# Optimization experiments

Hardware: AMD Instinct MI355X
Metric: run time of the kernel (lower is better)

Reference implementation:

```python
import jax, jax.numpy as jnp
import numpy as np

B, T, D, H, O = 1024, 512, 64, 64, 32


def setup_inputs() -> dict:
    key = jax.random.key(0)
    ks = jax.random.split(key, 12)
    s = 1.0 / np.sqrt(H)  # torch LSTM/Linear default init scale
    u = lambda k, shape: jax.random.uniform(k, shape, jnp.float32, -s, s)
    return {
        "x": jax.random.normal(ks[0], (B, T, D), jnp.float32),
        # layer 0 (PyTorch gate order: i, f, g, o stacked along first dim)
        "w_ih0": u(ks[1], (4 * H, D)),
        "w_hh0": u(ks[2], (4 * H, H)),
        "b_ih0": u(ks[3], (4 * H,)),
        "b_hh0": u(ks[4], (4 * H,)),
        # layer 1
        "w_ih1": u(ks[5], (4 * H, H)),
        "w_hh1": u(ks[6], (4 * H, H)),
        "b_ih1": u(ks[7], (4 * H,)),
        "b_hh1": u(ks[8], (4 * H,)),
        # final linear head
        "fc_w": u(ks[9], (O, H)),
        "fc_b": u(ks[10], (O,)),
    }


def lstm_layer(x, w_ih, w_hh, b_ih, b_hh):
    """Single batch-first LSTM layer, PyTorch gate order (i, f, g, o)."""
    Bb = x.shape[0]
    Hh = w_hh.shape[1]
    # precompute input contribution for all timesteps: (B, T, 4H)
    pre = jnp.einsum('btd,gd->btg', x, w_ih) + b_ih + b_hh

    def step(carry, p_t):  # p_t: (B, 4H)
        h, c = carry
        gates = p_t + h @ w_hh.T
        i, f, g, o = jnp.split(gates, 4, axis=-1)
        c = jax.nn.sigmoid(f) * c + jax.nn.sigmoid(i) * jnp.tanh(g)
        h = jax.nn.sigmoid(o) * jnp.tanh(c)
        return (h, c), h

    h0 = jnp.zeros((Bb, Hh), x.dtype)
    (_, _), hs = jax.lax.scan(step, (h0, h0), jnp.swapaxes(pre, 0, 1))
    return jnp.swapaxes(hs, 0, 1)  # (B, T, H)


def reference(x, w_ih0, w_hh0, b_ih0, b_hh0, w_ih1, w_hh1, b_ih1, b_hh1, fc_w, fc_b):
    h1 = lstm_layer(x, w_ih0, w_hh0, b_ih0, b_hh0)
    h2 = lstm_layer(h1, w_ih1, w_hh1, b_ih1, b_hh1)
    last = h2[:, -1, :]  # (B, H)
    return jax.nn.softplus(last @ fc_w.T + fc_b)  # (B, O)
```

## Files before the change

kernel.cpp:

```cpp
#include <hip/hip_runtime.h>
#include <math.h>

#define BB 1024
#define TT 512
#define OO 32
#define MM 4
#define NBLK (BB/MM)

typedef __attribute__((ext_vector_type(8))) short short8;
typedef __attribute__((ext_vector_type(4))) float f32x4;

#define MFMA __builtin_amdgcn_mfma_f32_16x16x32_bf16
#define LOG2E 1.4426950408889634f
#define K2    2.8853900817779268f

#define BAR() asm volatile("s_waitcnt lgkmcnt(0)\n\ts_barrier" ::: "memory")

__device__ __forceinline__ float exp2f_(float x) {
#if __has_builtin(__builtin_amdgcn_exp2f)
    return __builtin_amdgcn_exp2f(x);
#else
    float r; asm("v_exp_f32 %0, %1" : "=v"(r) : "v"(x)); return r;
#endif
}

__device__ __forceinline__ ushort f2bf(float f) {
    union { float f; unsigned u; } v; v.f = f;
    unsigned r = v.u + 0x7FFF + ((v.u >> 16) & 1);
    return (ushort)(r >> 16);
}
__device__ __forceinline__ float bf2f(ushort u) {
    union { unsigned u; float f; } v; v.u = ((unsigned)u) << 16; return v.f;
}
__device__ __forceinline__ unsigned pkbf(float a, float b) {
    union { float f; unsigned u; } x, y; x.f = a; y.f = b;
    return __builtin_amdgcn_perm(y.u + 0x8000u, x.u + 0x8000u, 0x07060302u);
}
__device__ __forceinline__ short8 pack8(const float4& a, const float4& b) {
    union { unsigned u[4]; short8 s; } r;
    r.u[0] = pkbf(a.x, a.y); r.u[1] = pkbf(a.z, a.w);
    r.u[2] = pkbf(b.x, b.y); r.u[3] = pkbf(b.z, b.w);
    return r.s;
}

__global__ __launch_bounds__(512)
void lstm_f256(const float* __restrict__ x,
               const float* __restrict__ w_ih0,
               const float* __restrict__ w_hh0,
               const float* __restrict__ b_ih0,
               const float* __restrict__ b_hh0,
               const float* __restrict__ w_ih1,
               const float* __restrict__ w_hh1,
               const float* __restrict__ b_ih1,
               const float* __restrict__ b_hh1,
               const float* __restrict__ fc_w,
               const float* __restrict__ fc_b,
               float* __restrict__ out)
{
    __shared__ __align__(16) ushort h0s[2][4][80];
    __shared__ __align__(16) ushort h1s[2][4][80];

    const int tid  = threadIdx.x;
    const int wv   = tid >> 6;
    const bool gB  = (wv >= 4);
    const int u    = wv & 3;
    const int ln   = tid & 63;
    const int l15  = ln & 15;
    const int quad = ln >> 4;
    const int b0   = blockIdx.x * MM;
    const int hq   = 16 * u + l15;
    const int xr   = l15 >> 2;

    const float* wih = gB ? w_ih1 : w_ih0;
    const float* whh = gB ? w_hh1 : w_hh0;
    const float* bih = gB ? b_ih1 : b_ih0;
    const float* bhh = gB ? b_hh1 : b_hh0;

    short8 bfrag[4][4];
    f32x4  bias4[4];
#pragma unroll
    for (int g = 0; g < 4; ++g) {
        const float sc = (g == 2) ? K2 : -LOG2E;
        const int col = 64 * g + 16 * u + l15;
        const float bv = (bih[col] + bhh[col]) * sc;
        bias4[g] = (f32x4){bv, bv, bv, bv};
#pragma unroll
        for (int kt = 0; kt < 4; ++kt) {
            const int kb = kt * 32 + quad * 8;
            const float* src = (kb < 64) ? (wih + col * 64 + kb)
                                         : (whh + col * 64 + (kb - 64));
            const float4 v0 = *(const float4*)src;
            const float4 v1 = *(const float4*)(src + 4);
            short8 b;
            b[0] = (short)f2bf(v0.x * sc); b[1] = (short)f2bf(v0.y * sc);
            b[2] = (short)f2bf(v0.z * sc); b[3] = (short)f2bf(v0.w * sc);
            b[4] = (short)f2bf(v1.x * sc); b[5] = (short)f2bf(v1.y * sc);
            b[6] = (short)f2bf(v1.z * sc); b[7] = (short)f2bf(v1.w * sc);
            bfrag[g][kt] = b;
        }
    }

    const size_t xoff = ((size_t)(b0 + xr) * TT) * 64 + quad * 8;
    float4 xfA0, xfA1, xfA2, xfA3, xfB0, xfB1, xfB2, xfB3;
    f32x4 pre[4];
    const f32x4 z4 = (f32x4){0.f, 0.f, 0.f, 0.f};

#define ISSUE(t_, S)                                                          \
    if ((t_) < TT) {                                                          \
        const float* p = x + xoff + (size_t)(t_) * 64;                        \
        xf##S##0 = *(const float4*)p;        xf##S##1 = *(const float4*)(p + 4);  \
        xf##S##2 = *(const float4*)(p + 32); xf##S##3 = *(const float4*)(p + 36); \
    }

    for (int i = tid; i < 2 * 4 * 80; i += 512) {
        ((ushort*)h0s)[i] = 0;
        ((ushort*)h1s)[i] = 0;
    }

    float cc = 0.f;
    if (!gB) {
        ISSUE(0, A);
        ISSUE(1, B);
        const short8 xlo = pack8(xfA0, xfA1);
        const short8 xhi = pack8(xfA2, xfA3);
#pragma unroll
        for (int g = 0; g < 4; ++g)
            pre[g] = MFMA(xhi, bfrag[g][1],
                          MFMA(xlo, bfrag[g][0], bias4[g], 0, 0, 0), 0, 0, 0);
    }
    BAR();

#define CELL1(YI, YF, YG, YO, HD, NXT)                                        \
    {                                                                         \
        const float Ef = exp2f_(YF);                                          \
        const float Ei = exp2f_(YI);                                          \
        const float Eg = exp2f_(fminf((YG), 80.f));                           \
        const float sf = __builtin_amdgcn_rcpf(1.f + Ef);                     \
        const float rd = __builtin_amdgcn_rcpf((1.f + Ei) * (1.f + Eg));      \
        cc = sf * cc + (Eg - 1.f) * rd;                                       \
        const float Ec = exp2f_(fminf(cc * K2, 80.f));                        \
        const float Eo = exp2f_(YO);                                          \
        const float r2 = __builtin_amdgcn_rcpf((1.f + Eo) * (1.f + Ec));      \
        union { float f; unsigned uu; } hv; hv.f = (Ec - 1.f) * r2;           \
        HD[NXT][quad][hq] = (ushort)((hv.uu + 0x8000u) >> 16);                \
    }

#define STEP(t_, CUR, NXT, USE, LD, DOA, DOB)                                 \
    {                                                                         \
        if (!gB) {                                                            \
            if (DOA) {                                                        \
                const short8 a2 = *(const short8*)&h0s[CUR][xr][quad * 8];    \
                const short8 a3 = *(const short8*)&h0s[CUR][xr][32 + quad * 8]; \
                f32x4 aA[4], aB[4];                                           \
                _Pragma("unroll")                                             \
                for (int g = 0; g < 4; ++g) {                                 \
                    aA[g] = MFMA(a2, bfrag[g][2], pre[g], 0, 0, 0);           \
                    aB[g] = MFMA(a3, bfrag[g][3], z4, 0, 0, 0);               \
                }                                                             \
                ISSUE((t_) + 2, LD);                                          \
                const float yi = aA[0][0] + aB[0][0];                         \
                const float yf = aA[1][0] + aB[1][0];                         \
                const float yg = aA[2][0] + aB[2][0];                         \
                const float yo = aA[3][0] + aB[3][0];                         \
                CELL1(yi, yf, yg, yo, h0s, NXT);                              \
                if ((t_) + 1 < TT) {                                          \
                    const short8 xlo = pack8(xf##USE##0, xf##USE##1);         \
                    const short8 xhi = pack8(xf##USE##2, xf##USE##3);         \
                    _Pragma("unroll")                                         \
                    for (int g = 0; g < 4; ++g)                               \
                        pre[g] = MFMA(xhi, bfrag[g][1],                       \
                                      MFMA(xlo, bfrag[g][0], bias4[g], 0,0,0), 0,0,0); \
                }                                                             \
            }                                                                 \
        } else {                                                              \
            if (DOB) {                                                        \
                const short8 a0 = *(const short8*)&h0s[CUR][xr][quad * 8];    \
                const short8 a1 = *(const short8*)&h0s[CUR][xr][32 + quad * 8]; \
                const short8 a2 = *(const short8*)&h1s[CUR][xr][quad * 8];    \
                const short8 a3 = *(const short8*)&h1s[CUR][xr][32 + quad * 8]; \
                f32x4 aA[4], aB[4];                                           \
                _Pragma("unroll")                                             \
                for (int g = 0; g < 4; ++g) {                                 \
                    aA[g] = MFMA(a1, bfrag[g][1],                             \
                                 MFMA(a0, bfrag[g][0], bias4[g], 0, 0, 0), 0, 0, 0); \
                    aB[g] = MFMA(a3, bfrag[g][3],                             \
                                 MFMA(a2, bfrag[g][2], z4, 0, 0, 0), 0, 0, 0); \
                }                                                             \
                const float yi = aA[0][0] + aB[0][0];                         \
                const float yf = aA[1][0] + aB[1][0];                         \
                const float yg = aA[2][0] + aB[2][0];                         \
                const float yo = aA[3][0] + aB[3][0];                         \
                CELL1(yi, yf, yg, yo, h1s, NXT);                              \
            }                                                                 \
        }                                                                     \
        BAR();                                                                \
    }

    STEP(0, 0, 1, B, A, 1, 0)
    for (int tb = 1; tb + 2 < TT; tb += 2) {
        STEP(tb,     1, 0, A, B, 1, 1)
        STEP(tb + 1, 0, 1, B, A, 1, 1)
    }
    STEP(TT - 1, 1, 0, A, B, 1, 1)
    STEP(TT, 0, 1, B, A, 0, 1)
#undef STEP
#undef CELL1
#undef ISSUE

    if (tid < MM * OO) {
        const int row = tid >> 5, o = tid & 31;
        float a = fc_b[o];
#pragma unroll
        for (int j = 0; j < 64; ++j)
            a = fmaf(fc_w[o * 64 + j], bf2f(h1s[1][row][j]), a);
        out[(size_t)(b0 + row) * OO + o] =
            fmaxf(a, 0.0f) + log1pf(__expf(-fabsf(a)));
    }
}

extern "C" void kernel_launch(void* const* d_in, const int* in_sizes, int n_in,
                              void* d_out, int out_size, void* d_ws, size_t ws_size,
                              hipStream_t stream) {
    const float* x     = (const float*)d_in[0];
    const float* w_ih0 = (const float*)d_in[1];
    const float* w_hh0 = (const float*)d_in[2];
    const float* b_ih0 = (const float*)d_in[3];
    const float* b_hh0 = (const float*)d_in[4];
    const float* w_ih1 = (const float*)d_in[5];
    const float* w_hh1 = (const float*)d_in[6];
    const float* b_ih1 = (const float*)d_in[7];
    const float* b_hh1 = (const float*)d_in[8];
    const float* fc_w  = (const float*)d_in[9];
    const float* fc_b  = (const float*)d_in[10];
    float* out = (float*)d_out;

    lstm_f256<<<dim3(NBLK), dim3(512), 0, stream>>>(
        x, w_ih0, w_hh0, b_ih0, b_hh0,
        w_ih1, w_hh1, b_ih1, b_hh1, fc_w, fc_b, out);
}
```

Measured before the change: 485.3 us.

## Split LSTM into recurrent and producer waves with chunked pre-activation pipeline

Restructures the kernel so that two waves run only the serial recurrences, one per layer, each computing all 64 hidden units with no block barrier per timestep. Two producer waves precompute the input projections for chunks of 8 timesteps into double-buffered shared memory. Layer 0's hidden states go into a 16-slot ring so the producer waves can compute layer 1's input projections one chunk behind. Barriers now happen once per chunk instead of once per step, which removes most synchronisation on the critical path. In exchange, each recurrent wave does four times more MFMA and cell work per step in a single wave, and the per-block LDS footprint grows sharply, which may limit occupancy.

```diff
diff --git a/kernel.cpp b/kernel.cpp
--- a/kernel.cpp
+++ b/kernel.cpp
@@ -6,6 +6,8 @@
 #define OO 32
 #define MM 4
 #define NBLK (BB/MM)
+#define SS 8
+#define NSLOT 66
 
 typedef __attribute__((ext_vector_type(8))) short short8;
 typedef __attribute__((ext_vector_type(4))) float f32x4;
@@ -43,176 +45,230 @@
     return r.s;
 }
 
-__global__ __launch_bounds__(512)
-void lstm_f256(const float* __restrict__ x,
-               const float* __restrict__ w_ih0,
-               const float* __restrict__ w_hh0,
-               const float* __restrict__ b_ih0,
-               const float* __restrict__ b_hh0,
-               const float* __restrict__ w_ih1,
-               const float* __restrict__ w_hh1,
-               const float* __restrict__ b_ih1,
-               const float* __restrict__ b_hh1,
-               const float* __restrict__ fc_w,
-               const float* __restrict__ fc_b,
-               float* __restrict__ out)
+__global__ __launch_bounds__(256, 1)
+void lstm_pc(const float* __restrict__ x,
+             const float* __restrict__ w_ih0,
+             const float* __restrict__ w_hh0,
+             const float* __restrict__ b_ih0,
+             const float* __restrict__ b_hh0,
+             const float* __restrict__ w_ih1,
+             const float* __restrict__ w_hh1,
+             const float* __restrict__ b_ih1,
+             const float* __restrict__ b_hh1,
+             const float* __restrict__ fc_w,
+             const float* __restrict__ fc_b,
+             float* __restrict__ out)
 {
-    __shared__ __align__(16) ushort h0s[2][4][80];
-    __shared__ __align__(16) ushort h1s[2][4][80];
-
-    const int tid  = threadIdx.x;
-    const int wv   = tid >> 6;
-    const bool gB  = (wv >= 4);
-    const int u    = wv & 3;
-    const int ln   = tid & 63;
-    const int l15  = ln & 15;
-    const int quad = ln >> 4;
-    const int b0   = blockIdx.x * MM;
-    const int hq   = 16 * u + l15;
-    const int xr   = l15 >> 2;
-
-    const float* wih = gB ? w_ih1 : w_ih0;
-    const float* whh = gB ? w_hh1 : w_hh0;
-    const float* bih = gB ? b_ih1 : b_ih0;
-    const float* bhh = gB ? b_hh1 : b_hh0;
-
-    short8 bfrag[4][4];
-    f32x4  bias4[4];
-#pragma unroll
-    for (int g = 0; g < 4; ++g) {
-        const float sc = (g == 2) ? K2 : -LOG2E;
-        const int col = 64 * g + 16 * u + l15;
-        const float bv = (bih[col] + bhh[col]) * sc;
-        bias4[g] = (f32x4){bv, bv, bv, bv};
-#pragma unroll
-        for (int kt = 0; kt < 4; ++kt) {
-            const int kb = kt * 32 + quad * 8;
-            const float* src = (kb < 64) ? (wih + col * 64 + kb)
-                                         : (whh + col * 64 + (kb - 64));
-            const float4 v0 = *(const float4*)src;
-            const float4 v1 = *(const float4*)(src + 4);
-            short8 b;
-            b[0] = (short)f2bf(v0.x * sc); b[1] = (short)f2bf(v0.y * sc);
-            b[2] = (short)f2bf(v0.z * sc); b[3] = (short)f2bf(v0.w * sc);
-            b[4] = (short)f2bf(v1.x * sc); b[5] = (short)f2bf(v1.y * sc);
-            b[6] = (short)f2bf(v1.z * sc); b[7] = (short)f2bf(v1.w * sc);
-            bfrag[g][kt] = b;
-        }
+    __shared__ float  pre0[2][SS][4][4][64];
+    __shared__ float  pre1[2][SS][4][4][64];
+    __shared__ ushort h0u[16][4][80];
+    __shared__ ushort h1u[2][4][80];
+
+    const int tid = threadIdx.x;
+    const int wv  = tid >> 6;
+    const int ln  = tid & 63;
+    const int l   = ln & 15;
+    const int q   = ln >> 4;
+    const int b0  = blockIdx.x * MM;
+    const f32x4 z4 = (f32x4){0.f, 0.f, 0.f, 0.f};
+
+    for (int i = tid; i < 16 * 4 * 80; i += 256) ((ushort*)h0u)[i] = 0;
+    for (int i = tid; i < 2 * 4 * 80;  i += 256) ((ushort*)h1u)[i] = 0;
+
+    if (wv < 2) {
+        const float* whh = wv ? w_hh1 : w_hh0;
+        short8 bf[4][4][2];
+#pragma unroll
+        for (int g = 0; g < 4; ++g) {
+            const float sc = (g == 2) ? K2 : -LOG2E;
+#pragma unroll
+            for (int c = 0; c < 4; ++c) {
+                const int col = 64 * g + 16 * c + l;
+#pragma unroll
+                for (int kt = 0; kt < 2; ++kt) {
+                    const float* src = whh + col * 64 + 32 * kt + 8 * q;
+                    const float4 v0 = *(const float4*)src;
+                    const float4 v1 = *(const float4*)(src + 4);
+                    short8 b;
+                    b[0] = (short)f2bf(v0.x * sc); b[1] = (short)f2bf(v0.y * sc);
+                    b[2] = (short)f2bf(v0.z * sc); b[3] = (short)f2bf(v0.w * sc);
+                    b[4] = (short)f2bf(v1.x * sc); b[5] = (short)f2bf(v1.y * sc);
+                    b[6] = (short)f2bf(v1.z * sc); b[7] = (short)f2bf(v1.w * sc);
+                    bf[g][c][kt] = b;
+                }
+            }
+        }
+        float cc[4] = {0.f, 0.f, 0.f, 0.f};
+        const int hrow = l >> 2;
+        const int hsw  = (16 * q) ^ (16 * hrow);
+        const float* preBase = wv ? &pre1[0][0][0][0][0] : &pre0[0][0][0][0][0];
+        char* ring = (char*)(wv ? (void*)h1u : (void*)h0u);
+        const int mask = wv ? 1 : 15;
+
+        for (int s = 0; s < NSLOT; ++s) {
+            BAR();
+            const bool act = wv ? (s >= 2) : (s < 64);
+            if (act) {
+                const int u_  = wv ? (s - 2) : s;
+                const int base_t = SS * u_;
+                const float* pb0 = preBase + (u_ & 1) * 8192 + q * 256;
+#pragma unroll
+                for (int tau = 0; tau < SS; ++tau) {
+                    const int t = base_t + tau;
+                    const char* hb = ring + ((t - 1) & mask) * 640 + hrow * 160;
+                    const short8 a0 = *(const short8*)(hb + hsw);
+                    const short8 a1 = *(const short8*)(hb + 64 + hsw);
+                    const float* pp = pb0 + tau * 1024;
+                    float y[4][4];
+#pragma unroll
+                    for (int g = 0; g < 4; ++g)
+#pragma unroll
+                        for (int w = 0; w < 4; ++w)
+                            y[g][w] = pp[g * 64 + ((16 * w + l) ^ (16 * q))];
+#pragma unroll
+                    for (int c = 0; c < 4; ++c)
+#pragma unroll
+                        for (int g = 0; g < 4; ++g) {
+                            f32x4 acc = MFMA(a1, bf[g][c][1],
+                                             MFMA(a0, bf[g][c][0], z4, 0, 0, 0),
+                                             0, 0, 0);
+                            y[g][c] += acc[0];
+                        }
+                    char* wb = ring + (t & mask) * 640 + q * 160;
+#pragma unroll
+                    for (int w = 0; w < 4; ++w) {
+                        const float y0 = y[0][w], y1 = y[1][w];
+                        const float y2 = y[2][w], y3 = y[3][w];
+                        const float Ef = exp2f_(y1);
+                        const float Ei = exp2f_(y0);
+                        const float Eg = exp2f_(fminf(y2, 80.f));
+                        const float sf = __builtin_amdgcn_rcpf(1.f + Ef);
+                        const float rd = __builtin_amdgcn_rcpf((1.f + Ei) * (1.f + Eg));
+                        cc[w] = sf * cc[w] + (Eg - 1.f) * rd;
+                        const float Ec = exp2f_(fminf(cc[w] * K2, 80.f));
+                        const float Eo = exp2f_(y3);
+                        const float r2 = __builtin_amdgcn_rcpf((1.f + Eo) * (1.f + Ec));
+                        union { float f; unsigned u; } hv; hv.f = (Ec - 1.f) * r2;
+                        const ushort hval = (ushort)((hv.u + 0x8000u) >> 16);
+                        *(ushort*)(wb + ((32 * w + 2 * l) ^ (16 * q))) = hval;
+                    }
+                }
+            }
+        }
+    } else {
+        const int c0 = 2 * (wv - 2);
+        short8 wi0[4][2][2], wi1[4][2][2];
+        float  bv0[4][2], bv1[4][2];
+#pragma unroll
+        for (int g = 0; g < 4; ++g) {
+            const float sc = (g == 2) ? K2 : -LOG2E;
+#pragma unroll
+            for (int ci = 0; ci < 2; ++ci) {
+                const int col = 64 * g + 16 * (c0 + ci) + l;
+                bv0[g][ci] = (b_ih0[col] + b_hh0[col]) * sc;
+                bv1[g][ci] = (b_ih1[col] + b_hh1[col]) * sc;
+#pragma unroll
+                for (int kt = 0; kt < 2; ++kt) {
+                    const int ko = 32 * kt + 8 * q;
+#define LDW(dst, W)                                                           \
+                    { const float4 v0 = *(const float4*)(W + col * 64 + ko);  \
+                      const float4 v1 = *(const float4*)(W + col * 64 + ko + 4); \
+                      short8 b;                                               \
+                      b[0]=(short)f2bf(v0.x*sc); b[1]=(short)f2bf(v0.y*sc);   \
+                      b[2]=(short)f2bf(v0.z*sc); b[3]=(short)f2bf(v0.w*sc);   \
+                      b[4]=(short)f2bf(v1.x*sc); b[5]=(short)f2bf(v1.y*sc);   \
+                      b[6]=(short)f2bf(v1.z*sc); b[7]=(short)f2bf(v1.w*sc);   \
+                      dst = b; }
+                    LDW(wi0[g][ci][kt], w_ih0)
+                    LDW(wi1[g][ci][kt], w_ih1)
+#undef LDW
+                }
+            }
+        }
+        const int xrow = l & 3, xtau = l >> 2;
+        const size_t xbase = ((size_t)(b0 + xrow) * TT) * 64 + 8 * q;
+
+#define COOP_PRE0(S_)                                                         \
+        {                                                                     \
+            const int buf = ((S_) + 1) & 1;                                   \
+            const int t0 = SS * ((S_) + 1);                                   \
+            float* dst0 = &pre0[buf][0][0][0][0];                             \
+            _Pragma("unroll")                                                 \
+            for (int hh = 0; hh < 2; ++hh) {                                  \
+                const float* px = x + xbase + (size_t)(t0 + 4 * hh + xtau) * 64; \
+                const float4 v0 = *(const float4*)px;                         \
+                const float4 v1 = *(const float4*)(px + 4);                   \
+                const float4 v2 = *(const float4*)(px + 32);                  \
+                const float4 v3 = *(const float4*)(px + 36);                  \
+                const short8 xa0 = pack8(v0, v1), xa1 = pack8(v2, v3);        \
+                _Pragma("unroll")                                             \
+                for (int ci = 0; ci < 2; ++ci)                                \
+                    _Pragma("unroll")                                         \
+                    for (int g = 0; g < 4; ++g) {                             \
+                        const float bv_ = bv0[g][ci];                         \
+                        f32x4 acc = (f32x4){bv_, bv_, bv_, bv_};              \
+                        acc = MFMA(xa0, wi0[g][ci][0], acc, 0, 0, 0);         \
+                        acc = MFMA(xa1, wi0[g][ci][1], acc, 0, 0, 0);         \
+                        const int uu = 16 * (c0 + ci) + l;                    \
+                        float* dd = dst0 + (4 * hh + q) * 1024 + g * 64;      \
+                        dd[0 * 256 + (uu ^ 0)]  = acc[0];                     \
+                        dd[1 * 256 + (uu ^ 16)] = acc[1];                     \
+                        dd[2 * 256 + (uu ^ 32)] = acc[2];                     \
+                        dd[3 * 256 + (uu ^ 48)] = acc[3];                     \
+                    }                                                         \
+            }                                                                 \
+        }
+
+#define COOP_PRE1(S_)                                                         \
+        {                                                                     \
+            const int buf = ((S_) - 1) & 1;                                   \
+            const int t1 = SS * ((S_) - 1);                                   \
+            float* dst1 = &pre1[buf][0][0][0][0];                             \
+            const int sw2 = (16 * q) ^ (16 * xrow);                           \
+            _Pragma("unroll")                                                 \
+            for (int hh = 0; hh < 2; ++hh) {                                  \
+                const int tt = t1 + 4 * hh + xtau;                            \
+                const char* hp = (const char*)h0u + (tt & 15) * 640 + xrow * 160; \
+                const short8 ha0 = *(const short8*)(hp + sw2);                \
+                const short8 ha1 = *(const short8*)(hp + 64 + sw2);           \
+                _Pragma("unroll")                                             \
+                for (int ci = 0; ci < 2; ++ci)                                \
+                    _Pragma("unroll")                                         \
+                    for (int g = 0; g < 4; ++g) {                             \
+                        const float bv_ = bv1[g][ci];                         \
+                        f32x4 acc = (f32x4){bv_, bv_, bv_, bv_};              \
+                        acc = MFMA(ha0, wi1[g][ci][0], acc, 0, 0, 0);         \
+                        acc = MFMA(ha1, wi1[g][ci][1], acc, 0, 0, 0);         \
+                        const int uu = 16 * (c0 + ci) + l;                    \
+                        float* dd = dst1 + (4 * hh + q) * 1024 + g * 64;      \
+                        dd[0 * 256 + (uu ^ 0)]  = acc[0];                     \
+                        dd[1 * 256 + (uu ^ 16)] = acc[1];                     \
+                        dd[2 * 256 + (uu ^ 32)] = acc[2];                     \
+                        dd[3 * 256 + (uu ^ 48)] = acc[3];                     \
+                    }                                                         \
+            }                                                                 \
+        }
+
+        COOP_PRE0(-1)
+        for (int s = 0; s < NSLOT; ++s) {
+            BAR();
+            if (s < 63) COOP_PRE0(s)
+            if (s >= 1 && s <= 64) COOP_PRE1(s)
+        }
+#undef COOP_PRE0
+#undef COOP_PRE1
     }
 
-    const size_t xoff = ((size_t)(b0 + xr) * TT) * 64 + quad * 8;
-    float4 xfA0, xfA1, xfA2, xfA3, xfB0, xfB1, xfB2, xfB3;
-    f32x4 pre[4];
-    const f32x4 z4 = (f32x4){0.f, 0.f, 0.f, 0.f};
-
-#define ISSUE(t_, S)                                                          \
-    if ((t_) < TT) {                                                          \
-        const float* p = x + xoff + (size_t)(t_) * 64;                        \
-        xf##S##0 = *(const float4*)p;        xf##S##1 = *(const float4*)(p + 4);  \
-        xf##S##2 = *(const float4*)(p + 32); xf##S##3 = *(const float4*)(p + 36); \
-    }
-
-    for (int i = tid; i < 2 * 4 * 80; i += 512) {
-        ((ushort*)h0s)[i] = 0;
-        ((ushort*)h1s)[i] = 0;
-    }
-
-    float cc = 0.f;
-    if (!gB) {
-        ISSUE(0, A);
-        ISSUE(1, B);
-        const short8 xlo = pack8(xfA0, xfA1);
-        const short8 xhi = pack8(xfA2, xfA3);
-#pragma unroll
-        for (int g = 0; g < 4; ++g)
-            pre[g] = MFMA(xhi, bfrag[g][1],
-                          MFMA(xlo, bfrag[g][0], bias4[g], 0, 0, 0), 0, 0, 0);
-    }
     BAR();
-
-#define CELL1(YI, YF, YG, YO, HD, NXT)                                        \
-    {                                                                         \
-        const float Ef = exp2f_(YF);                                          \
-        const float Ei = exp2f_(YI);                                          \
-        const float Eg = exp2f_(fminf((YG), 80.f));                           \
-        const float sf = __builtin_amdgcn_rcpf(1.f + Ef);                     \
-        const float rd = __builtin_amdgcn_rcpf((1.f + Ei) * (1.f + Eg));      \
-        cc = sf * cc + (Eg - 1.f) * rd;                                       \
-        const float Ec = exp2f_(fminf(cc * K2, 80.f));                        \
-        const float Eo = exp2f_(YO);                                          \
-        const float r2 = __builtin_amdgcn_rcpf((1.f + Eo) * (1.f + Ec));      \
-        union { float f; unsigned uu; } hv; hv.f = (Ec - 1.f) * r2;           \
-        HD[NXT][quad][hq] = (ushort)((hv.uu + 0x8000u) >> 16);                \
-    }
-
-#define STEP(t_, CUR, NXT, USE, LD, DOA, DOB)                                 \
-    {                                                                         \
-        if (!gB) {                                                            \
-            if (DOA) {                                                        \
-                const short8 a2 = *(const short8*)&h0s[CUR][xr][quad * 8];    \
-                const short8 a3 = *(const short8*)&h0s[CUR][xr][32 + quad * 8]; \
-                f32x4 aA[4], aB[4];                                           \
-                _Pragma("unroll")                                             \
-                for (int g = 0; g < 4; ++g) {                                 \
-                    aA[g] = MFMA(a2, bfrag[g][2], pre[g], 0, 0, 0);           \
-                    aB[g] = MFMA(a3, bfrag[g][3], z4, 0, 0, 0);               \
-                }                                                             \
-                ISSUE((t_) + 2, LD);                                          \
-                const float yi = aA[0][0] + aB[0][0];                         \
-                const float yf = aA[1][0] + aB[1][0];                         \
-                const float yg = aA[2][0] + aB[2][0];                         \
-                const float yo = aA[3][0] + aB[3][0];                         \
-                CELL1(yi, yf, yg, yo, h0s, NXT);                              \
-                if ((t_) + 1 < TT) {                                          \
-                    const short8 xlo = pack8(xf##USE##0, xf##USE##1);         \
-                    const short8 xhi = pack8(xf##USE##2, xf##USE##3);         \
-                    _Pragma("unroll")                                         \
-                    for (int g = 0; g < 4; ++g)                               \
-                        pre[g] = MFMA(xhi, bfrag[g][1],                       \
-                                      MFMA(xlo, bfrag[g][0], bias4[g], 0,0,0), 0,0,0); \
-                }                                                             \
-            }                                                                 \
-        } else {                                                              \
-            if (DOB) {                                                        \
-                const short8 a0 = *(const short8*)&h0s[CUR][xr][quad * 8];    \
-                const short8 a1 = *(const short8*)&h0s[CUR][xr][32 + quad * 8]; \
-                const short8 a2 = *(const short8*)&h1s[CUR][xr][quad * 8];    \
-                const short8 a3 = *(const short8*)&h1s[CUR][xr][32 + quad * 8]; \
-                f32x4 aA[4], aB[4];                                           \
-                _Pragma("unroll")                                             \
-                for (int g = 0; g < 4; ++g) {                                 \
-                    aA[g] = MFMA(a1, bfrag[g][1],                             \
-                                 MFMA(a0, bfrag[g][0], bias4[g], 0, 0, 0), 0, 0, 0); \
-                    aB[g] = MFMA(a3, bfrag[g][3],                             \
-                                 MFMA(a2, bfrag[g][2], z4, 0, 0, 0), 0, 0, 0); \
-                }                                                             \
-                const float yi = aA[0][0] + aB[0][0];                         \
-                const float yf = aA[1][0] + aB[1][0];                         \
-                const float yg = aA[2][0] + aB[2][0];                         \
-                const float yo = aA[3][0] + aB[3][0];                         \
-                CELL1(yi, yf, yg, yo, h1s, NXT);                              \
-            }                                                                 \
-        }                                                                     \
-        BAR();                                                                \
-    }
-
-    STEP(0, 0, 1, B, A, 1, 0)
-    for (int tb = 1; tb + 2 < TT; tb += 2) {
-        STEP(tb,     1, 0, A, B, 1, 1)
-        STEP(tb + 1, 0, 1, B, A, 1, 1)
-    }
-    STEP(TT - 1, 1, 0, A, B, 1, 1)
-    STEP(TT, 0, 1, B, A, 0, 1)
-#undef STEP
-#undef CELL1
-#undef ISSUE
-
     if (tid < MM * OO) {
         const int row = tid >> 5, o = tid & 31;
         float a = fc_b[o];
 #pragma unroll
-        for (int j = 0; j < 64; ++j)
-            a = fmaf(fc_w[o * 64 + j], bf2f(h1s[1][row][j]), a);
+        for (int j = 0; j < 64; ++j) {
+            const ushort hv = *(const ushort*)((const char*)h1u + 640
+                              + row * 160 + ((2 * j) ^ (16 * row)));
+            a = fmaf(fc_w[o * 64 + j], bf2f(hv), a);
+        }
         out[(size_t)(b0 + row) * OO + o] =
             fmaxf(a, 0.0f) + log1pf(__expf(-fabsf(a)));
     }
@@ -234,7 +290,7 @@
     const float* fc_b  = (const float*)d_in[10];
     float* out = (float*)d_out;
 
-    lstm_f256<<<dim3(NBLK), dim3(512), 0, stream>>>(
+    lstm_pc<<<dim3(NBLK), dim3(256), 0, stream>>>(
         x, w_ih0, w_hh0, b_ih0, b_hh0,
         w_ih1, w_hh1, b_ih1, b_hh1, fc_w, fc_b, out);
 }
```

Result: faster. 472.9 us (-2.6%).
